# Optimization experiments

Hardware: AMD Instinct MI355X
Metric: run time of the kernel (lower is better)

The kernel has to match this reference:

```python
import jax, jax.numpy as jnp
import numpy as np

# DREAMPlace IDXST_IDCT (a.k.a. idsct2): y[u,v] = sum_p sum_q x[p,q] * sin(pi*p*(u+0.5)/M) * cos(pi*q*(v+0.5)/N)
# i.e. IDXST (inverse discrete sine transform, DST-III-like, unnormalized) along the M axis
# and IDCT (DCT-III-like, unnormalized, full weight on k=0) along the N axis.
# Computed with the classic 2N-padded FFT trick using the precomputed twiddles
# expk[k] = exp(-1j*pi*k/(2N)) stored as [N,2] (real, imag), matching precompute_expk.

def _idxt_spectrum(x, expk):
    """F[u] = sum_k x[k] * exp(-1j*pi*k*(2u+1)/(2N)), along last axis.
    Re(F) is the IDCT sum (cos), -Im(F) is the IDXST sum (sin)."""
    N = x.shape[-1]
    c = (x * expk[..., 0]) + 1j * (x * expk[..., 1])  # x[k] * exp(-j*pi*k/(2N))
    z = jnp.concatenate([c, jnp.zeros_like(c)], axis=-1)  # zero-pad to 2N
    return jnp.fft.fft(z, axis=-1)[..., :N]


def idct_1d(x, expk):
    # y[u] = sum_k x[k] cos(pi*k*(2u+1)/(2N))
    return _idxt_spectrum(x, expk).real


def idxst_1d(x, expk):
    # y[u] = sum_k x[k] sin(pi*k*(2u+1)/(2N))
    return -_idxt_spectrum(x, expk).imag


def _make_expk(L):
    k = jnp.arange(L, dtype=jnp.float32) * (np.pi / (2.0 * L))
    return jnp.stack([jnp.cos(k), -jnp.sin(k)], axis=-1)  # exp(-j*pi*k/(2L))


def setup_inputs() -> dict:
    M, N = 4096, 4096
    key = jax.random.key(0)
    x = jax.random.normal(key, (M, N), dtype=jnp.float32)
    return {"x": x, "expkM": _make_expk(M), "expkN": _make_expk(N)}


def reference(x, expkM, expkN):
    # IDCT along the last dim (N), then IDXST along the second-to-last dim (M):
    # idxst(idct(x)^T)^T
    t = idct_1d(x, expkN)                                        # [M, N]
    y = idxst_1d(t.swapaxes(-2, -1), expkM).swapaxes(-2, -1)     # [M, N]
    return y
```

## Files before the change

### kernel.cpp

```cpp
#include <hip/hip_runtime.h>
#include <hip/hip_bf16.h>
#include <stdint.h>
#include <cmath>


typedef __attribute__((ext_vector_type(4))) float f32x4;
typedef __attribute__((ext_vector_type(8))) unsigned short u16x8;
typedef __attribute__((ext_vector_type(8))) __bf16 bf16x8;

__device__ __forceinline__ unsigned short f2bf(float f) {
  union { float f; unsigned u; } v; v.f = f;
  unsigned u = v.u + 0x7fffu + ((v.u >> 16) & 1u);
  return (unsigned short)(u >> 16);
}

__device__ __forceinline__ void gen_half(int idx, u16x8* Pe, u16x8* Po,
                                         int isSin, int jshift, int jmask,
                                         unsigned mask4L, float sc) {
  int i = idx >> jshift;
  int jb = (idx & jmask) * 8;
  unsigned tp = 2u * (unsigned)i + 1u;
  unsigned re = (2u * (unsigned)jb * tp) & mask4L;
  unsigned ro = (re + tp) & mask4L;
  unsigned step = (2u * tp) & mask4L;
  u16x8 pe, po;
#pragma unroll
  for (int t = 0; t < 8; t++) {
    float se_, ce_, so_, co_;
    __sincosf((float)re * sc, &se_, &ce_);
    __sincosf((float)ro * sc, &so_, &co_);
    pe[t] = f2bf(isSin ? se_ : ce_);
    po[t] = f2bf(isSin ? so_ : co_);
    re = (re + step) & mask4L;
    ro = (ro + step) & mask4L;
  }
  Pe[idx] = pe;
  Po[idx] = po;
}

__global__ void prep_kernel(const f32x4* __restrict__ x, u16x8* __restrict__ xe,
                            u16x8* __restrict__ xo, u16x8* __restrict__ Ce,
                            u16x8* __restrict__ Co, u16x8* __restrict__ Se,
                            u16x8* __restrict__ So, int nConvBlocks,
                            int nGenNBlocks, int jshiftN, int jmaskN,
                            unsigned mask4N, float scN, int jshiftM, int jmaskM,
                            unsigned mask4M, float scM) {
  int b = blockIdx.x;
  if (b < nConvBlocks) {
    int idx = b * 256 + threadIdx.x;
    f32x4 a = x[4 * idx], bb = x[4 * idx + 1], c = x[4 * idx + 2],
          d = x[4 * idx + 3];
    u16x8 e, o;
    e[0] = f2bf(a[0]);  o[0] = f2bf(a[1]);  e[1] = f2bf(a[2]);  o[1] = f2bf(a[3]);
    e[2] = f2bf(bb[0]); o[2] = f2bf(bb[1]); e[3] = f2bf(bb[2]); o[3] = f2bf(bb[3]);
    e[4] = f2bf(c[0]);  o[4] = f2bf(c[1]);  e[5] = f2bf(c[2]);  o[5] = f2bf(c[3]);
    e[6] = f2bf(d[0]);  o[6] = f2bf(d[1]);  e[7] = f2bf(d[2]);  o[7] = f2bf(d[3]);
    xe[idx] = e;
    xo[idx] = o;
  } else if (b < nConvBlocks + nGenNBlocks) {
    int idx = (b - nConvBlocks) * 256 + threadIdx.x;
    gen_half(idx, Ce, Co, 0, jshiftN, jmaskN, mask4N, scN);
  } else {
    int idx = (b - nConvBlocks - nGenNBlocks) * 256 + threadIdx.x;
    gen_half(idx, Se, So, 1, jshiftM, jmaskM, mask4M, scM);
  }
}

template <int STAGE>
__global__ __launch_bounds__(512, 2) void fused_gemm_kernel(
    const unsigned short* __restrict__ Ae,
    const unsigned short* __restrict__ Ao,
    const unsigned short* __restrict__ Be,
    const unsigned short* __restrict__ Bo,
    unsigned short* __restrict__ out0, unsigned short* __restrict__ out1,
    int outStride, int K, int Lfull) {
  __shared__ unsigned short AsE[128 * 64];
  __shared__ unsigned short BsE[256 * 64];
  __shared__ unsigned short AsO[128 * 64];
  __shared__ unsigned short BsO[256 * 64];

  const int tid = threadIdx.x;

  const int nwg = gridDim.x * gridDim.y;
  const int lin = blockIdx.y * gridDim.x + blockIdx.x;
  int swb = lin;
  if ((nwg & 7) == 0) swb = (lin & 7) * (nwg >> 3) + (lin >> 3);
  const int m0 = (swb / gridDim.x) * 128;
  const int n0 = (swb % gridDim.x) * 256;

  const int wave = tid >> 6;
  const int lane = tid & 63;
  const int wm = (wave >> 2) * 64;
  const int wn = (wave & 3) * 64;
  const int l16 = lane & 15;
  const int quad = lane >> 4;
  const int swz = (quad ^ (l16 & 7)) * 8;

  const int lrow = lane >> 3;
  const int lsw = ((lane & 7) ^ lrow) * 8;

  auto stage = [&](const unsigned short* __restrict__ A,
                   const unsigned short* __restrict__ B, unsigned short* As,
                   unsigned short* Bs, int k0) {
    const unsigned short* Ap =
        A + (size_t)(m0 + 8 * wave + lrow) * K + lsw + k0;
    const unsigned short* Bp =
        B + (size_t)(n0 + 8 * wave + lrow) * K + lsw + k0;
    unsigned short* Adst = As + wave * 512;
    unsigned short* Bdst = Bs + wave * 512;
#define GLL(src, dst)                                                        \
  __builtin_amdgcn_global_load_lds(                                          \
      (const __attribute__((address_space(1))) void*)(src),                  \
      (__attribute__((address_space(3))) void*)(dst), 16, 0, 0)
    GLL(Ap, Adst);
    GLL(Ap + (size_t)64 * K, Adst + 4096);
    GLL(Bp, Bdst);
    GLL(Bp + (size_t)64 * K, Bdst + 4096);
    GLL(Bp + (size_t)128 * K, Bdst + 8192);
    GLL(Bp + (size_t)192 * K, Bdst + 12288);
#undef GLL
  };

  f32x4 accE[4][4], accO[4][4];
#pragma unroll
  for (int i = 0; i < 4; i++)
#pragma unroll
    for (int j = 0; j < 4; j++) {
      accE[i][j] = f32x4{0.f, 0.f, 0.f, 0.f};
      accO[i][j] = f32x4{0.f, 0.f, 0.f, 0.f};
    }

  auto phase = [&](const unsigned short* As, const unsigned short* Bs,
                   f32x4 (&acc)[4][4]) {
#pragma unroll
    for (int h = 0; h < 2; h++) {
      const int so = swz ^ (h * 32);
      bf16x8 af[4], bfr[4];
#pragma unroll
      for (int i = 0; i < 4; i++)
        af[i] = *(const bf16x8*)(As + (wm + i * 16 + l16) * 64 + so);
#pragma unroll
      for (int j = 0; j < 4; j++)
        bfr[j] = *(const bf16x8*)(Bs + (wn + j * 16 + l16) * 64 + so);
#pragma unroll
      for (int i = 0; i < 4; i++)
#pragma unroll
        for (int j = 0; j < 4; j++)
          acc[i][j] = __builtin_amdgcn_mfma_f32_16x16x32_bf16(
              af[i], bfr[j], acc[i][j], 0, 0, 0);
    }
  };

  stage(Ae, Be, AsE, BsE, 0);
  __syncthreads();

  for (int k0 = 0; k0 < K; k0 += 64) {
    stage(Ao, Bo, AsO, BsO, k0);
    phase(AsE, BsE, accE);
    __syncthreads();
    if (k0 + 64 < K) stage(Ae, Be, AsE, BsE, k0 + 64);
    phase(AsO, BsO, accO);
    __syncthreads();
  }

#pragma unroll
  for (int i = 0; i < 4; i++) {
#pragma unroll
    for (int j = 0; j < 4; j++) {
      int n = n0 + wn + j * 16 + l16;
      int mb = m0 + wm + i * 16 + quad * 4;
#pragma unroll
      for (int r = 0; r < 4; r++) {
        float e = accE[i][j][r];
        float o = accO[i][j][r];
        int m = mb + r;
        if (STAGE == 1) {
          unsigned short* mat = (n & 1) ? out1 : out0;
          int c = n >> 1;
          mat[(size_t)m * outStride + c] = f2bf(e + o);
          mat[(size_t)(Lfull - 1 - m) * outStride + c] = f2bf(e - o);
        } else {
          float* y = (float*)out0;
          y[(size_t)m * outStride + n] = e + o;
          y[(size_t)(Lfull - 1 - m) * outStride + n] = o - e;
        }
      }
    }
  }
}

extern "C" void kernel_launch(void* const* d_in, const int* in_sizes, int n_in,
                              void* d_out, int out_size, void* d_ws,
                              size_t ws_size, hipStream_t stream) {
  const float* x = (const float*)d_in[0];
  const int M = in_sizes[1] / 2;
  const int N = in_sizes[2] / 2;
  const size_t MN = (size_t)M * N;

  unsigned short* ws = (unsigned short*)d_ws;
  unsigned short* xe = ws;
  unsigned short* xo = ws + MN / 2;
  unsigned short* Ce = ws + MN;
  unsigned short* Co = ws + MN + MN / 4;
  unsigned short* Se = ws + MN * 3 / 2;
  unsigned short* So = ws + MN * 7 / 4;
  unsigned short* tTe = ws + MN * 2;
  unsigned short* tTo = ws + MN * 5 / 2;

  int shiftN = 0; while ((1 << shiftN) < N) shiftN++;
  int shiftM = 0; while ((1 << shiftM) < M) shiftM++;

  int nConvBlocks = (int)(MN / 16 / 256);
  int nGenNBlocks = (N / 2) * (N / 2) / 8 / 256;
  int nGenMBlocks = (M / 2) * (M / 2) / 8 / 256;
  prep_kernel<<<nConvBlocks + nGenNBlocks + nGenMBlocks, 256, 0, stream>>>(
      (const f32x4*)x, (u16x8*)xe, (u16x8*)xo, (u16x8*)Ce, (u16x8*)Co,
      (u16x8*)Se, (u16x8*)So, nConvBlocks, nGenNBlocks, shiftN - 4,
      (N / 16) - 1, (unsigned)(4 * N - 1),
      (float)(3.14159265358979323846 / (2.0 * N)), shiftM - 4, (M / 16) - 1,
      (unsigned)(4 * M - 1), (float)(3.14159265358979323846 / (2.0 * M)));

  fused_gemm_kernel<1><<<dim3(M / 256, (N / 2) / 128), 512, 0, stream>>>(
      Ce, Co, xe, xo, tTe, tTo, M / 2, N / 2, N);

  fused_gemm_kernel<2><<<dim3(N / 256, (M / 2) / 128), 512, 0, stream>>>(
      Se, So, tTe, tTo, (unsigned short*)d_out, nullptr, N, M / 2, M);
}
```

Before: 270.4 us.

## Restructure GEMM main loop with explicit vmcnt waits, split phases, and MFMA priority

Replaces the __syncthreads-based double buffer with a schedule that issues both even and odd stage loads up front. It then uses explicit s_waitcnt vmcnt(6)/lgkmcnt(0) with sched barriers and raw s_barrier, so one buffer's global-to-LDS loads stay in flight while the other is computed. Each phase is split into two half-K steps separated by barriers, and s_setprio raises priority around the MFMA bursts. The goal is to overlap memory with compute and to avoid full vmcnt(0) drains. The cost is more barriers per iteration, plus reliance on hand-tuned wait counts that must match the six loads issued per stage.

```diff
diff --git a/kernel.cpp b/kernel.cpp
--- a/kernel.cpp
+++ b/kernel.cpp
@@ -66,6 +66,23 @@
   }
 }
 
+#define LGKM0()                                             \
+  do {                                                      \
+    asm volatile("s_waitcnt lgkmcnt(0)" ::: "memory");      \
+    __builtin_amdgcn_sched_barrier(0);                      \
+  } while (0)
+#define VMCNT6()                                            \
+  do {                                                      \
+    asm volatile("s_waitcnt vmcnt(6)" ::: "memory");        \
+    __builtin_amdgcn_sched_barrier(0);                      \
+  } while (0)
+#define VMCNT0()                                            \
+  do {                                                      \
+    asm volatile("s_waitcnt vmcnt(0)" ::: "memory");        \
+    __builtin_amdgcn_sched_barrier(0);                      \
+  } while (0)
+#define BAR() __builtin_amdgcn_s_barrier()
+
 template <int STAGE>
 __global__ __launch_bounds__(512, 2) void fused_gemm_kernel(
     const unsigned short* __restrict__ Ae,
@@ -130,37 +147,58 @@
       accO[i][j] = f32x4{0.f, 0.f, 0.f, 0.f};
     }
 
-  auto phase = [&](const unsigned short* As, const unsigned short* Bs,
-                   f32x4 (&acc)[4][4]) {
-#pragma unroll
-    for (int h = 0; h < 2; h++) {
-      const int so = swz ^ (h * 32);
-      bf16x8 af[4], bfr[4];
-#pragma unroll
-      for (int i = 0; i < 4; i++)
-        af[i] = *(const bf16x8*)(As + (wm + i * 16 + l16) * 64 + so);
+  auto phase_h = [&](const unsigned short* As, const unsigned short* Bs,
+                     int h, f32x4 (&acc)[4][4]) {
+    const int so = swz ^ (h * 32);
+    bf16x8 af[4], bfr[4];
+#pragma unroll
+    for (int i = 0; i < 4; i++)
+      af[i] = *(const bf16x8*)(As + (wm + i * 16 + l16) * 64 + so);
+#pragma unroll
+    for (int j = 0; j < 4; j++)
+      bfr[j] = *(const bf16x8*)(Bs + (wn + j * 16 + l16) * 64 + so);
+    LGKM0();
+    __builtin_amdgcn_s_setprio(1);
+#pragma unroll
+    for (int i = 0; i < 4; i++)
 #pragma unroll
       for (int j = 0; j < 4; j++)
-        bfr[j] = *(const bf16x8*)(Bs + (wn + j * 16 + l16) * 64 + so);
-#pragma unroll
-      for (int i = 0; i < 4; i++)
-#pragma unroll
-        for (int j = 0; j < 4; j++)
-          acc[i][j] = __builtin_amdgcn_mfma_f32_16x16x32_bf16(
-              af[i], bfr[j], acc[i][j], 0, 0, 0);
-    }
+        acc[i][j] = __builtin_amdgcn_mfma_f32_16x16x32_bf16(
+            af[i], bfr[j], acc[i][j], 0, 0, 0);
+    __builtin_amdgcn_s_setprio(0);
   };
 
   stage(Ae, Be, AsE, BsE, 0);
-  __syncthreads();
+  stage(Ao, Bo, AsO, BsO, 0);
+  VMCNT6();
+  BAR();
 
   for (int k0 = 0; k0 < K; k0 += 64) {
-    stage(Ao, Bo, AsO, BsO, k0);
-    phase(AsE, BsE, accE);
-    __syncthreads();
-    if (k0 + 64 < K) stage(Ae, Be, AsE, BsE, k0 + 64);
-    phase(AsO, BsO, accO);
-    __syncthreads();
+    const bool lastIt = (k0 + 64 >= K);
+
+    phase_h(AsE, BsE, 0, accE);
+    BAR();
+    phase_h(AsE, BsE, 1, accE);
+    BAR();
+    if (!lastIt) {
+      stage(Ae, Be, AsE, BsE, k0 + 64);
+      VMCNT6();
+    } else {
+      VMCNT0();
+    }
+    BAR();
+
+    phase_h(AsO, BsO, 0, accO);
+    BAR();
+    phase_h(AsO, BsO, 1, accO);
+    BAR();
+    if (!lastIt) {
+      stage(Ao, Bo, AsO, BsO, k0 + 64);
+      VMCNT6();
+    } else {
+      VMCNT0();
+    }
+    BAR();
   }
 
 #pragma unroll
```

New measurement: 292.4 us. 1.08x slower.
